# Kernel optimization log

Hardware: AMD Instinct MI355X
Metric: run time of the kernel (lower is better)

## Reference

```python
import jax, jax.numpy as jnp
import numpy as np

QUANT = 6                      # quant bits
LEVELS = 2 ** QUANT - 1        # quant_levels = 63


def setup_inputs() -> dict:
    key = jax.random.key(0)
    k1, k2, k3 = jax.random.split(key, 3)
    B, C_in, C_out, H, W = 8, 256, 256, 64, 64
    x = jax.random.normal(k1, (B, C_in, H, W), dtype=jnp.float32)
    # 1x1 conv weight stored as [out_channels, in_channels] (kernel dims are 1)
    weight = jax.random.normal(k2, (C_out, C_in), dtype=jnp.float32) * 0.05
    bias = jax.random.normal(k3, (C_out,), dtype=jnp.float32) * 0.05
    return {"x": x, "weight": weight, "bias": bias}


def reference(x, weight, bias):
    """NoiseConv.forward with hard_weight set, mode='batch':
    channel_wise_quantize -> hardware_inference -> float cast.
    (Original computes in float64 on CUDA; here float32 for jit/accel friendliness.)
    """
    # --- channel_wise_quantize (input is detached in torch) ---
    xd = jax.lax.stop_gradient(x)
    cmax = jnp.max(xd, axis=1, keepdims=True)           # [B,1,H,W]
    cmin = jnp.min(xd, axis=1, keepdims=True)           # [B,1,H,W]
    scaling = (cmax - cmin) / LEVELS                    # [B,1,H,W]
    x_int = jnp.round((xd - cmin) / scaling).astype(jnp.int32)  # [B,C,H,W] in [0,63]
    bit_idx = jnp.arange(QUANT, dtype=jnp.int32)
    bits = ((x_int[..., None] >> bit_idx) & 1).astype(x.dtype)   # [B,C,H,W,Q] bitplanes

    # --- hardware_inference (batch mode): one 1x1 conv per bitplane, then
    # weighted recombination with 2^b. Fused here into a single einsum; the
    # math is identical since conv is linear and bitplane values are exact. ---
    base = (2.0 ** jnp.arange(QUANT)).astype(x.dtype)   # quant_base
    out_sum = jnp.einsum('bchwq,q,oc->bohw', bits, base, weight)  # [B,O,H,W]
    out_w = out_sum * scaling                           # per-pixel rescale

    # min-offset term: conv2d(cmin * ones_like(x_plane), weight, bias).
    # cmin is constant across input channels, so it equals cmin * sum_c(w) + bias.
    wsum = jnp.sum(weight, axis=1)                      # [O]
    out_w = out_w + cmin * wsum[None, :, None, None] + bias[None, :, None, None]

    return out_w.astype(jnp.float32)
```

## Files before the change

### kernel.cpp

```cpp
#include <hip/hip_runtime.h>
#include <stdint.h>

#define CI 256
#define CO 256
#define HW 4096
#define PT 64
#define QPAD 72

typedef __attribute__((ext_vector_type(8))) short short8;
typedef __attribute__((ext_vector_type(4))) float float4v;

__global__ void prep_kernel(const float* __restrict__ w,
                            ushort* __restrict__ w16,
                            float* __restrict__ wsum) {
    const int o = blockIdx.x;
    const int lane = threadIdx.x;
    float4 v = ((const float4*)(w + o * CI))[lane];
    auto cvt = [](float f) -> ushort {
        uint32_t u = __float_as_uint(f);
        return (ushort)((u + 0x7FFFu + ((u >> 16) & 1u)) >> 16);
    };
    ushort4 q;
    q.x = cvt(v.x); q.y = cvt(v.y); q.z = cvt(v.z); q.w = cvt(v.w);
    ((ushort4*)(w16 + o * CI))[lane] = q;
    float s = v.x + v.y + v.z + v.w;
    for (int off = 32; off >= 1; off >>= 1) s += __shfl_down(s, off);
    if (lane == 0) wsum[o] = s;
}

__global__ __launch_bounds__(256, 2)
void noise_conv_kernel(const float* __restrict__ x,
                       const ushort* __restrict__ w16,
                       const float* __restrict__ wsum,
                       const float* __restrict__ bias,
                       float* __restrict__ out) {
    __shared__ ushort Qlds[PT][QPAD];
    __shared__ float4 rmin4[16][16];
    __shared__ float4 rmax4[16][16];
    __shared__ float cmin_s[PT], s_s[PT], inv_s[PT];

    const int t = threadIdx.x;
    const int blk = blockIdx.x;
    const int img = blk >> 6;
    const int p0 = (blk & 63) * PT;
    const float* xb = x + (size_t)img * CI * HW + p0;
    float* outb = out + (size_t)img * CO * HW + p0;

    {
        const int pg = t & 15;
        const int slice = t >> 4;
        float4 vmin = make_float4(__builtin_inff(), __builtin_inff(),
                                  __builtin_inff(), __builtin_inff());
        float4 vmax = make_float4(-__builtin_inff(), -__builtin_inff(),
                                  -__builtin_inff(), -__builtin_inff());
        #pragma unroll
        for (int i = 0; i < 16; ++i) {
            const float4 v = ((const float4*)(xb + (size_t)(slice * 16 + i) * HW))[pg];
            vmin.x = fminf(vmin.x, v.x); vmax.x = fmaxf(vmax.x, v.x);
            vmin.y = fminf(vmin.y, v.y); vmax.y = fmaxf(vmax.y, v.y);
            vmin.z = fminf(vmin.z, v.z); vmax.z = fmaxf(vmax.z, v.z);
            vmin.w = fminf(vmin.w, v.w); vmax.w = fmaxf(vmax.w, v.w);
        }
        rmin4[slice][pg] = vmin;
        rmax4[slice][pg] = vmax;
    }
    __syncthreads();
    if (t < 16) {
        float4 mn = rmin4[0][t], mx = rmax4[0][t];
        for (int sl = 1; sl < 16; ++sl) {
            float4 a = rmin4[sl][t], b = rmax4[sl][t];
            mn.x = fminf(mn.x, a.x); mx.x = fmaxf(mx.x, b.x);
            mn.y = fminf(mn.y, a.y); mx.y = fmaxf(mx.y, b.y);
            mn.z = fminf(mn.z, a.z); mx.z = fmaxf(mx.z, b.z);
            mn.w = fminf(mn.w, a.w); mx.w = fmaxf(mx.w, b.w);
        }
        const float mnv[4] = {mn.x, mn.y, mn.z, mn.w};
        const float mxv[4] = {mx.x, mx.y, mx.z, mx.w};
        #pragma unroll
        for (int c = 0; c < 4; ++c) {
            const int p = t * 4 + c;
            const float cmin = mnv[c];
            const float sc = (mxv[c] - cmin) / 63.0f;
            cmin_s[p] = cmin;
            s_s[p] = sc;
            inv_s[p] = 1.0f / sc;
        }
    }
    __syncthreads();

    const int lane = t & 63;
    const int wv = t >> 6;
    const int row16 = lane & 15;
    const int quad = lane >> 4;

    float4v acc[4][4];
    #pragma unroll
    for (int m = 0; m < 4; ++m)
        #pragma unroll
        for (int n = 0; n < 4; ++n) {
            float4v z = {0.0f, 0.0f, 0.0f, 0.0f};
            acc[m][n] = z;
        }

    const int sp = t & 63;
    const int scb = (t >> 6) * 16;
    const float cm = cmin_s[sp];
    const float iv = inv_s[sp];

    for (int c0 = 0; c0 < CI; c0 += 64) {
        #pragma unroll
        for (int jj = 0; jj < 2; ++jj) {
            uint32_t wds[4];
            #pragma unroll
            for (int j2 = 0; j2 < 4; ++j2) {
                const int c = c0 + scb + jj * 8 + j2 * 2;
                const float a0 = xb[(size_t)c * HW + sp];
                const float a1 = xb[(size_t)(c + 1) * HW + sp];
                const float q0 = rintf((a0 - cm) * iv);
                const float q1 = rintf((a1 - cm) * iv);
                const uint32_t b0 = __float_as_uint(q0) >> 16;
                const uint32_t b1 = __float_as_uint(q1) >> 16;
                wds[j2] = b0 | (b1 << 16);
            }
            *((uint4*)&Qlds[sp][scb + jj * 8]) =
                make_uint4(wds[0], wds[1], wds[2], wds[3]);
        }
        __syncthreads();

        #pragma unroll
        for (int ks = 0; ks < 2; ++ks) {
            const int kk = ks * 32 + quad * 8;
            short8 afr[4], bfr[4];
            #pragma unroll
            for (int m = 0; m < 4; ++m) {
                const int o = wv * 64 + m * 16 + row16;
                afr[m] = *((const short8*)(w16 + o * CI + c0 + kk));
            }
            #pragma unroll
            for (int n = 0; n < 4; ++n) {
                bfr[n] = *((const short8*)&Qlds[n * 16 + row16][kk]);
            }
            #pragma unroll
            for (int m = 0; m < 4; ++m)
                #pragma unroll
                for (int n = 0; n < 4; ++n)
                    acc[m][n] = __builtin_amdgcn_mfma_f32_16x16x32_bf16(
                        afr[m], bfr[n], acc[m][n], 0, 0, 0);
        }
        __syncthreads();
    }

    #pragma unroll
    for (int m = 0; m < 4; ++m) {
        const int ob = wv * 64 + m * 16 + quad * 4;
        const float4 w4 = *((const float4*)(wsum + ob));
        const float4 b4 = *((const float4*)(bias + ob));
        const float wr[4] = {w4.x, w4.y, w4.z, w4.w};
        const float br[4] = {b4.x, b4.y, b4.z, b4.w};
        #pragma unroll
        for (int n = 0; n < 4; ++n) {
            const int pl = n * 16 + row16;
            const float sc = s_s[pl];
            const float cm2 = cmin_s[pl];
            float* op = outb + pl;
            #pragma unroll
            for (int r = 0; r < 4; ++r) {
                op[(size_t)(ob + r) * HW] =
                    acc[m][n][r] * sc + cm2 * wr[r] + br[r];
            }
        }
    }
}

extern "C" void kernel_launch(void* const* d_in, const int* in_sizes, int n_in,
                              void* d_out, int out_size, void* d_ws, size_t ws_size,
                              hipStream_t stream) {
    const float* x    = (const float*)d_in[0];
    const float* w    = (const float*)d_in[1];
    const float* bias = (const float*)d_in[2];
    float* out = (float*)d_out;

    ushort* w16 = (ushort*)d_ws;
    float* wsum = (float*)((char*)d_ws + (size_t)CO * CI * sizeof(ushort));

    prep_kernel<<<CO, 64, 0, stream>>>(w, w16, wsum);
    noise_conv_kernel<<<512, 256, 0, stream>>>(x, w16, wsum, bias, out);
}
```

Measured before the change: 99.30 us.

## Load x once into registers, quantize full K tile into LDS, use 512 threads

```diff
diff --git a/kernel.cpp b/kernel.cpp
--- a/kernel.cpp
+++ b/kernel.cpp
@@ -5,10 +5,14 @@
 #define CO 256
 #define HW 4096
 #define PT 64
-#define QPAD 72
+#define QP 264
 
 typedef __attribute__((ext_vector_type(8))) short short8;
 typedef __attribute__((ext_vector_type(4))) float float4v;
+
+__device__ __forceinline__ float fcomp(const float4& v, int c) {
+    return c == 0 ? v.x : c == 1 ? v.y : c == 2 ? v.z : v.w;
+}
 
 __global__ void prep_kernel(const float* __restrict__ w,
                             ushort* __restrict__ w16,
@@ -28,15 +32,15 @@
     if (lane == 0) wsum[o] = s;
 }
 
-__global__ __launch_bounds__(256, 2)
+__global__ __launch_bounds__(512, 4)
 void noise_conv_kernel(const float* __restrict__ x,
                        const ushort* __restrict__ w16,
                        const float* __restrict__ wsum,
                        const float* __restrict__ bias,
                        float* __restrict__ out) {
-    __shared__ ushort Qlds[PT][QPAD];
-    __shared__ float4 rmin4[16][16];
-    __shared__ float4 rmax4[16][16];
+    __shared__ ushort Qlds[PT][QP];
+    __shared__ float4 wmin[8][16];
+    __shared__ float4 wmax[8][16];
     __shared__ float cmin_s[PT], s_s[PT], inv_s[PT];
 
     const int t = threadIdx.x;
@@ -46,113 +50,108 @@
     const float* xb = x + (size_t)img * CI * HW + p0;
     float* outb = out + (size_t)img * CO * HW + p0;
 
-    {
-        const int pg = t & 15;
-        const int slice = t >> 4;
-        float4 vmin = make_float4(__builtin_inff(), __builtin_inff(),
-                                  __builtin_inff(), __builtin_inff());
-        float4 vmax = make_float4(-__builtin_inff(), -__builtin_inff(),
-                                  -__builtin_inff(), -__builtin_inff());
+    const int pg = t & 15;
+    const int slice = t >> 4;
+
+    float4 xv[8];
+    #pragma unroll
+    for (int i = 0; i < 8; ++i)
+        xv[i] = ((const float4*)(xb + (size_t)(slice * 8 + i) * HW))[pg];
+
+    float4 vmin = xv[0], vmax = xv[0];
+    #pragma unroll
+    for (int i = 1; i < 8; ++i) {
+        vmin.x = fminf(vmin.x, xv[i].x); vmax.x = fmaxf(vmax.x, xv[i].x);
+        vmin.y = fminf(vmin.y, xv[i].y); vmax.y = fmaxf(vmax.y, xv[i].y);
+        vmin.z = fminf(vmin.z, xv[i].z); vmax.z = fmaxf(vmax.z, xv[i].z);
+        vmin.w = fminf(vmin.w, xv[i].w); vmax.w = fmaxf(vmax.w, xv[i].w);
+    }
+    #pragma unroll
+    for (int off = 16; off <= 32; off <<= 1) {
+        vmin.x = fminf(vmin.x, __shfl_xor(vmin.x, off));
+        vmin.y = fminf(vmin.y, __shfl_xor(vmin.y, off));
+        vmin.z = fminf(vmin.z, __shfl_xor(vmin.z, off));
+        vmin.w = fminf(vmin.w, __shfl_xor(vmin.w, off));
+        vmax.x = fmaxf(vmax.x, __shfl_xor(vmax.x, off));
+        vmax.y = fmaxf(vmax.y, __shfl_xor(vmax.y, off));
+        vmax.z = fmaxf(vmax.z, __shfl_xor(vmax.z, off));
+        vmax.w = fmaxf(vmax.w, __shfl_xor(vmax.w, off));
+    }
+    const int wv = t >> 6;
+    if ((t & 63) < 16) { wmin[wv][pg] = vmin; wmax[wv][pg] = vmax; }
+    __syncthreads();
+
+    if (t < 64) {
+        const int g = t >> 2, c = t & 3;
+        float mn = fcomp(wmin[0][g], c), mx = fcomp(wmax[0][g], c);
         #pragma unroll
-        for (int i = 0; i < 16; ++i) {
-            const float4 v = ((const float4*)(xb + (size_t)(slice * 16 + i) * HW))[pg];
-            vmin.x = fminf(vmin.x, v.x); vmax.x = fmaxf(vmax.x, v.x);
-            vmin.y = fminf(vmin.y, v.y); vmax.y = fmaxf(vmax.y, v.y);
-            vmin.z = fminf(vmin.z, v.z); vmax.z = fmaxf(vmax.z, v.z);
-            vmin.w = fminf(vmin.w, v.w); vmax.w = fmaxf(vmax.w, v.w);
+        for (int w = 1; w < 8; ++w) {
+            mn = fminf(mn, fcomp(wmin[w][g], c));
+            mx = fmaxf(mx, fcomp(wmax[w][g], c));
         }
-        rmin4[slice][pg] = vmin;
-        rmax4[slice][pg] = vmax;
+        const float sc = (mx - mn) / 63.0f;
+        cmin_s[t] = mn;
+        s_s[t] = sc;
+        inv_s[t] = 1.0f / sc;
     }
     __syncthreads();
-    if (t < 16) {
-        float4 mn = rmin4[0][t], mx = rmax4[0][t];
-        for (int sl = 1; sl < 16; ++sl) {
-            float4 a = rmin4[sl][t], b = rmax4[sl][t];
-            mn.x = fminf(mn.x, a.x); mx.x = fmaxf(mx.x, b.x);
-            mn.y = fminf(mn.y, a.y); mx.y = fmaxf(mx.y, b.y);
-            mn.z = fminf(mn.z, a.z); mx.z = fmaxf(mx.z, b.z);
-            mn.w = fminf(mn.w, a.w); mx.w = fmaxf(mx.w, b.w);
+
+    {
+        float cm[4], iv[4];
+        #pragma unroll
+        for (int c2 = 0; c2 < 4; ++c2) {
+            cm[c2] = cmin_s[pg * 4 + c2];
+            iv[c2] = inv_s[pg * 4 + c2];
         }
-        const float mnv[4] = {mn.x, mn.y, mn.z, mn.w};
-        const float mxv[4] = {mx.x, mx.y, mx.z, mx.w};
         #pragma unroll
-        for (int c = 0; c < 4; ++c) {
-            const int p = t * 4 + c;
-            const float cmin = mnv[c];
-            const float sc = (mxv[c] - cmin) / 63.0f;
-            cmin_s[p] = cmin;
-            s_s[p] = sc;
-            inv_s[p] = 1.0f / sc;
+        for (int c2 = 0; c2 < 4; ++c2) {
+            uint32_t wds[4];
+            #pragma unroll
+            for (int j = 0; j < 4; ++j) {
+                const float q0 = rintf((fcomp(xv[2 * j],     c2) - cm[c2]) * iv[c2]);
+                const float q1 = rintf((fcomp(xv[2 * j + 1], c2) - cm[c2]) * iv[c2]);
+                wds[j] = (__float_as_uint(q0) >> 16) | (__float_as_uint(q1) & 0xFFFF0000u);
+            }
+            *((uint4*)&Qlds[pg * 4 + c2][slice * 8]) =
+                make_uint4(wds[0], wds[1], wds[2], wds[3]);
         }
     }
     __syncthreads();
 
     const int lane = t & 63;
-    const int wv = t >> 6;
     const int row16 = lane & 15;
     const int quad = lane >> 4;
 
-    float4v acc[4][4];
+    float4v acc[2][4];
     #pragma unroll
-    for (int m = 0; m < 4; ++m)
+    for (int m = 0; m < 2; ++m)
         #pragma unroll
         for (int n = 0; n < 4; ++n) {
             float4v z = {0.0f, 0.0f, 0.0f, 0.0f};
             acc[m][n] = z;
         }
 
-    const int sp = t & 63;
-    const int scb = (t >> 6) * 16;
-    const float cm = cmin_s[sp];
-    const float iv = inv_s[sp];
-
-    for (int c0 = 0; c0 < CI; c0 += 64) {
+    const ushort* wrow = w16 + (size_t)(wv * 32 + row16) * CI;
+    #pragma unroll
+    for (int ks = 0; ks < 8; ++ks) {
+        const int kk = ks * 32 + quad * 8;
+        short8 afr[2], bfr[4];
+        afr[0] = *((const short8*)(wrow + kk));
+        afr[1] = *((const short8*)(wrow + 16 * CI + kk));
         #pragma unroll
-        for (int jj = 0; jj < 2; ++jj) {
-            uint32_t wds[4];
+        for (int n = 0; n < 4; ++n)
+            bfr[n] = *((const short8*)&Qlds[n * 16 + row16][kk]);
+        #pragma unroll
+        for (int m = 0; m < 2; ++m)
             #pragma unroll
-            for (int j2 = 0; j2 < 4; ++j2) {
-                const int c = c0 + scb + jj * 8 + j2 * 2;
-                const float a0 = xb[(size_t)c * HW + sp];
-                const float a1 = xb[(size_t)(c + 1) * HW + sp];
-                const float q0 = rintf((a0 - cm) * iv);
-                const float q1 = rintf((a1 - cm) * iv);
-                const uint32_t b0 = __float_as_uint(q0) >> 16;
-                const uint32_t b1 = __float_as_uint(q1) >> 16;
-                wds[j2] = b0 | (b1 << 16);
-            }
-            *((uint4*)&Qlds[sp][scb + jj * 8]) =
-                make_uint4(wds[0], wds[1], wds[2], wds[3]);
-        }
-        __syncthreads();
-
-        #pragma unroll
-        for (int ks = 0; ks < 2; ++ks) {
-            const int kk = ks * 32 + quad * 8;
-            short8 afr[4], bfr[4];
-            #pragma unroll
-            for (int m = 0; m < 4; ++m) {
-                const int o = wv * 64 + m * 16 + row16;
-                afr[m] = *((const short8*)(w16 + o * CI + c0 + kk));
-            }
-            #pragma unroll
-            for (int n = 0; n < 4; ++n) {
-                bfr[n] = *((const short8*)&Qlds[n * 16 + row16][kk]);
-            }
-            #pragma unroll
-            for (int m = 0; m < 4; ++m)
-                #pragma unroll
-                for (int n = 0; n < 4; ++n)
-                    acc[m][n] = __builtin_amdgcn_mfma_f32_16x16x32_bf16(
-                        afr[m], bfr[n], acc[m][n], 0, 0, 0);
-        }
-        __syncthreads();
+            for (int n = 0; n < 4; ++n)
+                acc[m][n] = __builtin_amdgcn_mfma_f32_16x16x32_bf16(
+                    afr[m], bfr[n], acc[m][n], 0, 0, 0);
     }
 
     #pragma unroll
-    for (int m = 0; m < 4; ++m) {
-        const int ob = wv * 64 + m * 16 + quad * 4;
+    for (int m = 0; m < 2; ++m) {
+        const int ob = wv * 32 + m * 16 + quad * 4;
         const float4 w4 = *((const float4*)(wsum + ob));
         const float4 b4 = *((const float4*)(bias + ob));
         const float wr[4] = {w4.x, w4.y, w4.z, w4.w};
@@ -184,5 +183,5 @@
     float* wsum = (float*)((char*)d_ws + (size_t)CO * CI * sizeof(ushort));
 
     prep_kernel<<<CO, 64, 0, stream>>>(w, w16, wsum);
-    noise_conv_kernel<<<512, 256, 0, stream>>>(x, w16, wsum, bias, out);
+    noise_conv_kernel<<<512, 512, 0, stream>>>(x, w16, wsum, bias, out);
 }
```

After: 95.54 us. 3.8% less time.
